# Optimization experiments

Measured on AMD Instinct MI355X. Metric: run time of the kernel, lower is better.

## Reference

```python
import jax, jax.numpy as jnp
import numpy as np

K = 25          # kernel_size (number of B-spline control points)
DEGREE = 1      # open linear B-spline -> 2 nonzero basis weights per edge
N_NODES = 200000
N_EDGES = 6400000


def setup_inputs() -> dict:
    key = jax.random.key(0)
    k1, k2, k3, k4 = jax.random.split(key, 4)
    x = jax.random.normal(k1, (N_NODES, 2), dtype=jnp.float32)
    weight = jax.random.normal(k2, (K, 2, 1), dtype=jnp.float32)
    edges = jax.random.randint(k3, (2, N_EDGES), 0, N_NODES, dtype=jnp.int64)
    pseudo = jax.random.uniform(k4, (N_EDGES, 1), dtype=jnp.float32)
    return {"x": x, "weight": weight, "edges": edges, "pseudo": pseudo}


def reference(x, weight, edges, pseudo):
    # spline_conv with norm=True, no root_weight, no bias (forward only passes
    # x, edges, pseudo, weight, kernel_size=[25], is_open_spline=[1], degree, norm).
    row, col = edges[0], edges[1]   # messages gathered from col, scattered to row
    n = x.shape[0]

    # --- B-spline basis (open, degree 1, 1-D pseudo) ---
    p = pseudo[:, 0]                      # [E]
    v = p * (K - DEGREE)                  # [E], in [0, K-1)
    lo = jnp.floor(v)
    frac = v - lo                         # [E]
    i0 = jnp.clip(lo.astype(jnp.int32), 0, K - 1)       # [E]
    i1 = jnp.clip(i0 + 1, 0, K - 1)                     # [E]

    # --- gather + weighting: msg_e = sum_s basis[e,s] * x[col_e] @ W[idx[e,s]] ---
    xj = x[col]                                         # [E, 2]
    m0 = jnp.einsum('ef,efo->eo', xj, weight[i0])       # [E, 1]
    m1 = jnp.einsum('ef,efo->eo', xj, weight[i1])       # [E, 1]
    msg = (1.0 - frac)[:, None] * m0 + frac[:, None] * m1   # [E, 1]

    # --- scatter-add to target nodes ---
    out = jax.ops.segment_sum(msg, row, num_segments=n)     # [N, 1]

    # --- degree normalization (norm=True) ---
    deg = jax.ops.segment_sum(jnp.ones_like(p), row, num_segments=n)  # [N]
    out = out / jnp.clip(deg, 1.0, None)[:, None]
    return out
```

## Files before the change

### kernel.cpp

```cpp
#include <hip/hip_runtime.h>

#define KK 25
#define FP_SCALE 268435456.0f
#define FP_INV   (1.0f / 268435456.0f)

#define TPB 256
#define EPT 16
#define EPB (TPB * EPT)
#define WSHIFT 10
#define WNODE 1024
#define MAXBINS 256
#define CAP 36864
#define GSTRIDE 16

typedef unsigned long long u64;

__global__ void zero_counts(unsigned* __restrict__ p, int n) {
    int i = blockIdx.x * blockDim.x + threadIdx.x;
    if (i < n) p[i] = 0u;
}

__device__ __forceinline__ float2 ldg_l2(const float2* p) {
    u64 raw = __hip_atomic_load((const u64*)p, __ATOMIC_RELAXED,
                                __HIP_MEMORY_SCOPE_AGENT);
    union { u64 u; float2 f; } cv;
    cv.u = raw;
    return cv.f;
}

__global__ __launch_bounds__(TPB, 4) void phase1(
    const float* __restrict__ x,
    const float* __restrict__ w,
    const int* __restrict__ row,
    const int* __restrict__ col,
    const float* __restrict__ pseudo,
    unsigned* __restrict__ bucket,
    unsigned* __restrict__ gcount,
    int n_edges)
{
    __shared__ float4  wq[32];
    __shared__ unsigned bin_cnt[MAXBINS];
    __shared__ unsigned bin_start[MAXBINS];
    __shared__ unsigned joff[MAXBINS];
    __shared__ unsigned wtot[4];
    __shared__ unsigned stage[EPB];
    __shared__ unsigned char bin_map[EPB];

    const int tid = threadIdx.x;
    if (tid < KK) {
        int i1 = min(tid + 1, KK - 1);
        wq[tid] = make_float4(w[2 * tid], w[2 * tid + 1],
                              w[2 * i1],  w[2 * i1 + 1]);
    }
    bin_cnt[tid] = 0u;
    __syncthreads();

    const long long base = (long long)blockIdx.x * EPB;
    const bool full = (base + EPB) <= (long long)n_edges;
    const int nloc = full ? EPB
                          : (int)(((long long)n_edges - base) > 0
                                      ? ((long long)n_edges - base) : 0LL);

    unsigned entry[EPT];
    unsigned binrank[EPT];
    const float2* __restrict__ x2 = (const float2*)x;
    if (full) {
        const int4*   r4 = (const int4*)&row[base + (long long)tid * EPT];
        const int4*   c4 = (const int4*)&col[base + (long long)tid * EPT];
        const float4* p4 = (const float4*)&pseudo[base + (long long)tid * EPT];
        int4   rr[4], cc[4];
        float4 pp[4];
        #pragma unroll
        for (int q = 0; q < 4; ++q) { cc[q] = c4[q]; }
        float2 xj[16];
        #pragma unroll
        for (int q = 0; q < 4; ++q) {
            xj[4 * q + 0] = ldg_l2(&x2[cc[q].x]);
            xj[4 * q + 1] = ldg_l2(&x2[cc[q].y]);
            xj[4 * q + 2] = ldg_l2(&x2[cc[q].z]);
            xj[4 * q + 3] = ldg_l2(&x2[cc[q].w]);
        }
        #pragma unroll
        for (int q = 0; q < 4; ++q) { rr[q] = r4[q]; pp[q] = p4[q]; }
        int   ra[16];
        float pa[16];
        #pragma unroll
        for (int q = 0; q < 4; ++q) {
            ra[4 * q + 0] = rr[q].x; ra[4 * q + 1] = rr[q].y;
            ra[4 * q + 2] = rr[q].z; ra[4 * q + 3] = rr[q].w;
            pa[4 * q + 0] = pp[q].x; pa[4 * q + 1] = pp[q].y;
            pa[4 * q + 2] = pp[q].z; pa[4 * q + 3] = pp[q].w;
        }
        unsigned rk[16];
        #pragma unroll
        for (int k = 0; k < EPT; ++k) {
            int bin = ra[k] >> WSHIFT;
            rk[k] = atomicAdd(&bin_cnt[bin], 1u);
        }
        #pragma unroll
        for (int k = 0; k < EPT; ++k) {
            float vv = pa[k] * (float)(KK - 1);
            int   i0 = (int)vv;
            float fr = vv - (float)i0;
            float4 qw = wq[i0];
            float wa = qw.x + fr * (qw.z - qw.x);
            float wb = qw.y + fr * (qw.w - qw.y);
            float msg = xj[k].x * wa + xj[k].y * wb;
            unsigned ub = (__float_as_uint(msg) + 0x200u) & 0xFFFFFC00u;
            entry[k]   = ub | (unsigned)(ra[k] & (WNODE - 1));
            binrank[k] = ((unsigned)(ra[k] >> WSHIFT) << 12) | rk[k];
        }
    } else {
        for (int k = 0; k < EPT; ++k) {
            int i = tid * EPT + k;
            if (i < nloc) {
                long long e = base + i;
                int r = row[e];
                int c = col[e];
                float ps = pseudo[e];
                int bin = r >> WSHIFT;
                unsigned rank = atomicAdd(&bin_cnt[bin], 1u);
                float vv = ps * (float)(KK - 1);
                int   i0 = (int)vv;
                float fr = vv - (float)i0;
                float4 qw = wq[i0];
                float2 xj = ldg_l2(&x2[c]);
                float wa = qw.x + fr * (qw.z - qw.x);
                float wb = qw.y + fr * (qw.w - qw.y);
                float msg = xj.x * wa + xj.y * wb;
                unsigned ub = (__float_as_uint(msg) + 0x200u) & 0xFFFFFC00u;
                entry[k]   = ub | (unsigned)(r & (WNODE - 1));
                binrank[k] = ((unsigned)bin << 12) | rank;
            } else {
                binrank[k] = 0xFFFFFFFFu;
            }
        }
    }
    __syncthreads();

    {
        unsigned v = bin_cnt[tid];
        unsigned incl = v;
        #pragma unroll
        for (int d = 1; d < 64; d <<= 1) {
            unsigned t = __shfl_up(incl, d, 64);
            if ((tid & 63) >= d) incl += t;
        }
        if ((tid & 63) == 63) wtot[tid >> 6] = incl;
        __syncthreads();
        unsigned off = 0;
        const int wv = tid >> 6;
        #pragma unroll
        for (int ww = 0; ww < 4; ++ww)
            if (ww < wv) off += wtot[ww];
        unsigned st = off + incl - v;
        bin_start[tid] = st;
        unsigned gb = v ? atomicAdd(&gcount[tid * GSTRIDE], v) : 0u;
        joff[tid] = gb - st;
    }
    __syncthreads();

    if (full) {
        #pragma unroll
        for (int k = 0; k < EPT; ++k) {
            unsigned br  = binrank[k];
            unsigned bin = br >> 12;
            unsigned pos = bin_start[bin] + (br & 0xFFFu);
            stage[pos] = entry[k];
            bin_map[pos] = (unsigned char)bin;
        }
    } else {
        for (int k = 0; k < EPT; ++k) {
            unsigned br = binrank[k];
            if (br != 0xFFFFFFFFu) {
                unsigned bin = br >> 12;
                unsigned pos = bin_start[bin] + (br & 0xFFFu);
                stage[pos] = entry[k];
                bin_map[pos] = (unsigned char)bin;
            }
        }
    }
    __syncthreads();

    for (int i = tid; i < nloc; i += TPB) {
        unsigned e = stage[i];
        unsigned b = bin_map[i];
        unsigned g = joff[b] + (unsigned)i;
        if (g < CAP) bucket[(size_t)b * CAP + g] = e;
    }
}

__global__ __launch_bounds__(1024) void phase2(
    const unsigned* __restrict__ bucket,
    const unsigned* __restrict__ gcount,
    float* __restrict__ out, int n_nodes)
{
    __shared__ u64 acc[WNODE];
    const int tid = threadIdx.x;
    const int bin = blockIdx.x;

    acc[tid] = 0ULL;
    __syncthreads();

    unsigned cnt = gcount[bin * GSTRIDE];
    if (cnt > CAP) cnt = CAP;
    const unsigned* __restrict__ bb = bucket + (size_t)bin * CAP;

    const unsigned nvec = cnt >> 2;
    const uint4* __restrict__ b4 = (const uint4*)bb;

    for (unsigned chunk = 0; chunk < nvec; chunk += 8192u) {
        uint4 v[8];
        bool  hv[8];
        #pragma unroll
        for (int t = 0; t < 8; ++t) {
            unsigned i = chunk + (unsigned)tid + (unsigned)t * 1024u;
            hv[t] = (i < nvec);
            if (hv[t]) v[t] = b4[i];
        }
        #pragma unroll
        for (int t = 0; t < 8; ++t) {
            if (hv[t]) {
                unsigned ee[4] = {v[t].x, v[t].y, v[t].z, v[t].w};
                #pragma unroll
                for (int j = 0; j < 4; ++j) {
                    unsigned e = ee[j];
                    float msg = __uint_as_float(e & 0xFFFFFC00u);
                    long long fx = (long long)llrintf(msg * FP_SCALE);
                    atomicAdd(&acc[e & (WNODE - 1)], ((u64)fx << 16) | 1ULL);
                }
            }
        }
    }
    for (unsigned i = (nvec << 2) + tid; i < cnt; i += 1024) {
        unsigned e = bb[i];
        float msg = __uint_as_float(e & 0xFFFFFC00u);
        long long fx = (long long)llrintf(msg * FP_SCALE);
        atomicAdd(&acc[e & (WNODE - 1)], ((u64)fx << 16) | 1ULL);
    }
    __syncthreads();

    const int node = (bin << WSHIFT) + tid;
    if (node < n_nodes) {
        u64 t = acc[tid];
        int count = (int)(t & 0xFFFFULL);
        long long sf = ((long long)t) >> 16;
        float sum = (float)sf * FP_INV;
        out[node] = sum / (float)max(count, 1);
    }
}

__global__ void zero_acc(u64* __restrict__ p, int n) {
    int i = blockIdx.x * blockDim.x + threadIdx.x;
    if (i < n) p[i] = 0ULL;
}

__global__ void edge_kernel_flat(const float* __restrict__ x,
                                 const float* __restrict__ w,
                                 const int* __restrict__ row,
                                 const int* __restrict__ col,
                                 const float* __restrict__ pseudo,
                                 u64* __restrict__ acc,
                                 int n_edges) {
    __shared__ float wsm[KK * 2];
    if (threadIdx.x < KK * 2) wsm[threadIdx.x] = w[threadIdx.x];
    __syncthreads();

    const float2* __restrict__ x2 = (const float2*)x;
    int e = blockIdx.x * blockDim.x + threadIdx.x;
    if (e >= n_edges) return;

    int r = row[e];
    int c = col[e];
    float p = pseudo[e];
    float vv = p * (float)(KK - 1);
    float lo = floorf(vv);
    float fr = vv - lo;
    int i0 = min(max((int)lo, 0), KK - 1);
    int i1 = min(i0 + 1, KK - 1);
    float2 xj = x2[c];
    float m0 = xj.x * wsm[2 * i0] + xj.y * wsm[2 * i0 + 1];
    float m1 = xj.x * wsm[2 * i1] + xj.y * wsm[2 * i1 + 1];
    float msg = (1.0f - fr) * m0 + fr * m1;

    long long fx = (long long)llrintf(msg * FP_SCALE);
    atomicAdd(&acc[r], ((u64)fx << 16) + 1ULL);
}

__global__ void finalize_flat(const u64* __restrict__ acc,
                              float* __restrict__ out, int n) {
    int i = blockIdx.x * blockDim.x + threadIdx.x;
    if (i >= n) return;
    u64 t = acc[i];
    int count = (int)(t & 0xFFFFULL);
    long long sf = ((long long)t) >> 16;
    float sum = (float)sf * FP_INV;
    out[i] = sum / (float)max(count, 1);
}

extern "C" void kernel_launch(void* const* d_in, const int* in_sizes, int n_in,
                              void* d_out, int out_size, void* d_ws, size_t ws_size,
                              hipStream_t stream) {
    const float* x      = (const float*)d_in[0];
    const float* w      = (const float*)d_in[1];
    const int*   edges  = (const int*)d_in[2];
    const float* pseudo = (const float*)d_in[3];

    const int n_edges = in_sizes[3];
    const int n_nodes = out_size;

    const int* row = edges;
    const int* col = edges + n_edges;

    const int nbins = (n_nodes + WNODE - 1) >> WSHIFT;
    const size_t GBYTES = (size_t)MAXBINS * GSTRIDE * sizeof(unsigned);
    const size_t need = GBYTES + (size_t)nbins * CAP * sizeof(unsigned);

    if (nbins <= MAXBINS && ws_size >= need) {
        unsigned* gcount = (unsigned*)d_ws;
        unsigned* bucket = (unsigned*)((char*)d_ws + GBYTES);

        zero_counts<<<(MAXBINS * GSTRIDE + 255) / 256, 256, 0, stream>>>(
            gcount, MAXBINS * GSTRIDE);

        int blocks = (n_edges + EPB - 1) / EPB;
        phase1<<<blocks, TPB, 0, stream>>>(x, w, row, col, pseudo,
                                           bucket, gcount, n_edges);

        phase2<<<nbins, 1024, 0, stream>>>(bucket, gcount,
                                           (float*)d_out, n_nodes);
    } else {
        u64* acc = (u64*)d_ws;
        zero_acc<<<(n_nodes + 255) / 256, 256, 0, stream>>>(acc, n_nodes);
        int blocks = (n_edges + 255) / 256;
        edge_kernel_flat<<<blocks, 256, 0, stream>>>(x, w, row, col, pseudo,
                                                     acc, n_edges);
        finalize_flat<<<(n_nodes + 255) / 256, 256, 0, stream>>>(acc,
                                                                 (float*)d_out,
                                                                 n_nodes);
    }
}
```

Measured before the change: 162.4 us.

## Double phase1 block size and coalesce edge loads across lanes

Phase1 blocks grow from 256 to 512 threads, so each block bins 8192 edges and the rank field widens to 13 bits. The bin-scan code is guarded so only the first 256 threads touch per-bin state. Edge loads change from each thread reading 16 contiguous edges to a lane-interleaved int4 layout, so a wavefront's vector loads are contiguous across lanes. Larger blocks also mean fewer global atomic bucket reservations per edge, at the cost of more LDS per block and a different occupancy hint.

```diff
diff --git a/kernel.cpp b/kernel.cpp
--- a/kernel.cpp
+++ b/kernel.cpp
@@ -4,7 +4,7 @@
 #define FP_SCALE 268435456.0f
 #define FP_INV   (1.0f / 268435456.0f)
 
-#define TPB 256
+#define TPB 512
 #define EPT 16
 #define EPB (TPB * EPT)
 #define WSHIFT 10
@@ -12,6 +12,7 @@
 #define MAXBINS 256
 #define CAP 36864
 #define GSTRIDE 16
+#define RANKBITS 13
 
 typedef unsigned long long u64;
 
@@ -28,7 +29,7 @@
     return cv.f;
 }
 
-__global__ __launch_bounds__(TPB, 4) void phase1(
+__global__ __launch_bounds__(TPB, 6) void phase1(
     const float* __restrict__ x,
     const float* __restrict__ w,
     const int* __restrict__ row,
@@ -47,12 +48,14 @@
     __shared__ unsigned char bin_map[EPB];
 
     const int tid = threadIdx.x;
+    const int l   = tid & 63;
+    const int wv8 = tid >> 6;
     if (tid < KK) {
         int i1 = min(tid + 1, KK - 1);
         wq[tid] = make_float4(w[2 * tid], w[2 * tid + 1],
                               w[2 * i1],  w[2 * i1 + 1]);
     }
-    bin_cnt[tid] = 0u;
+    if (tid < MAXBINS) bin_cnt[tid] = 0u;
     __syncthreads();
 
     const long long base = (long long)blockIdx.x * EPB;
@@ -65,13 +68,15 @@
     unsigned binrank[EPT];
     const float2* __restrict__ x2 = (const float2*)x;
     if (full) {
-        const int4*   r4 = (const int4*)&row[base + (long long)tid * EPT];
-        const int4*   c4 = (const int4*)&col[base + (long long)tid * EPT];
-        const float4* p4 = (const float4*)&pseudo[base + (long long)tid * EPT];
+        const long long b4i = base >> 2;
+        const int i4 = wv8 * 256 + l;
+        const int4*   rp = (const int4*)row;
+        const int4*   cp = (const int4*)col;
+        const float4* qp = (const float4*)pseudo;
         int4   rr[4], cc[4];
         float4 pp[4];
         #pragma unroll
-        for (int q = 0; q < 4; ++q) { cc[q] = c4[q]; }
+        for (int q = 0; q < 4; ++q) { cc[q] = cp[b4i + i4 + 64 * q]; }
         float2 xj[16];
         #pragma unroll
         for (int q = 0; q < 4; ++q) {
@@ -81,7 +86,10 @@
             xj[4 * q + 3] = ldg_l2(&x2[cc[q].w]);
         }
         #pragma unroll
-        for (int q = 0; q < 4; ++q) { rr[q] = r4[q]; pp[q] = p4[q]; }
+        for (int q = 0; q < 4; ++q) {
+            rr[q] = rp[b4i + i4 + 64 * q];
+            pp[q] = qp[b4i + i4 + 64 * q];
+        }
         int   ra[16];
         float pa[16];
         #pragma unroll
@@ -108,11 +116,12 @@
             float msg = xj[k].x * wa + xj[k].y * wb;
             unsigned ub = (__float_as_uint(msg) + 0x200u) & 0xFFFFFC00u;
             entry[k]   = ub | (unsigned)(ra[k] & (WNODE - 1));
-            binrank[k] = ((unsigned)(ra[k] >> WSHIFT) << 12) | rk[k];
+            binrank[k] = ((unsigned)(ra[k] >> WSHIFT) << RANKBITS) | rk[k];
         }
     } else {
         for (int k = 0; k < EPT; ++k) {
-            int i = tid * EPT + k;
+            int q = k >> 2, j = k & 3;
+            int i = (wv8 * 256 + q * 64 + l) * 4 + j;
             if (i < nloc) {
                 long long e = base + i;
                 int r = row[e];
@@ -130,7 +139,7 @@
                 float msg = xj.x * wa + xj.y * wb;
                 unsigned ub = (__float_as_uint(msg) + 0x200u) & 0xFFFFFC00u;
                 entry[k]   = ub | (unsigned)(r & (WNODE - 1));
-                binrank[k] = ((unsigned)bin << 12) | rank;
+                binrank[k] = ((unsigned)bin << RANKBITS) | rank;
             } else {
                 binrank[k] = 0xFFFFFFFFu;
             }
@@ -139,24 +148,26 @@
     __syncthreads();
 
     {
-        unsigned v = bin_cnt[tid];
+        unsigned v = (tid < MAXBINS) ? bin_cnt[tid] : 0u;
         unsigned incl = v;
         #pragma unroll
         for (int d = 1; d < 64; d <<= 1) {
             unsigned t = __shfl_up(incl, d, 64);
             if ((tid & 63) >= d) incl += t;
         }
-        if ((tid & 63) == 63) wtot[tid >> 6] = incl;
+        if ((tid & 63) == 63 && tid < MAXBINS) wtot[tid >> 6] = incl;
         __syncthreads();
-        unsigned off = 0;
-        const int wv = tid >> 6;
-        #pragma unroll
-        for (int ww = 0; ww < 4; ++ww)
-            if (ww < wv) off += wtot[ww];
-        unsigned st = off + incl - v;
-        bin_start[tid] = st;
-        unsigned gb = v ? atomicAdd(&gcount[tid * GSTRIDE], v) : 0u;
-        joff[tid] = gb - st;
+        if (tid < MAXBINS) {
+            unsigned off = 0;
+            const int wvi = tid >> 6;
+            #pragma unroll
+            for (int ww = 0; ww < 4; ++ww)
+                if (ww < wvi) off += wtot[ww];
+            unsigned st = off + incl - v;
+            bin_start[tid] = st;
+            unsigned gb = v ? atomicAdd(&gcount[tid * GSTRIDE], v) : 0u;
+            joff[tid] = gb - st;
+        }
     }
     __syncthreads();
 
@@ -164,8 +175,8 @@
         #pragma unroll
         for (int k = 0; k < EPT; ++k) {
             unsigned br  = binrank[k];
-            unsigned bin = br >> 12;
-            unsigned pos = bin_start[bin] + (br & 0xFFFu);
+            unsigned bin = br >> RANKBITS;
+            unsigned pos = bin_start[bin] + (br & ((1u << RANKBITS) - 1u));
             stage[pos] = entry[k];
             bin_map[pos] = (unsigned char)bin;
         }
@@ -173,8 +184,8 @@
         for (int k = 0; k < EPT; ++k) {
             unsigned br = binrank[k];
             if (br != 0xFFFFFFFFu) {
-                unsigned bin = br >> 12;
-                unsigned pos = bin_start[bin] + (br & 0xFFFu);
+                unsigned bin = br >> RANKBITS;
+                unsigned pos = bin_start[bin] + (br & ((1u << RANKBITS) - 1u));
                 stage[pos] = entry[k];
                 bin_map[pos] = (unsigned char)bin;
             }
```

New measurement: 172.5 us. 6.2% more time.
